# Performance work log

Measured on AMD Instinct MI355X. Metric: run time of the kernel, lower is better.

## Reference

```python
import jax, jax.numpy as jnp
import numpy as np

B, C_IN, C_OUT, F, K = 4, 64, 64, 50000, 16
BN_EPS = 1e-5


def setup_inputs() -> dict:
    key = jax.random.key(0)
    k1, k2, k3, k4 = jax.random.split(key, 4)
    fea = jax.random.normal(k1, (B, C_IN, F), dtype=jnp.float32)
    ring_n = jax.random.randint(k2, (B, F, K), 0, F, dtype=jnp.int64)
    # Conv1d(kernel_size=1) weight [out, in] and bias [out]
    W = jax.random.normal(k3, (C_OUT, C_IN), dtype=jnp.float32) / np.sqrt(C_IN)
    b = jax.random.normal(k4, (C_OUT,), dtype=jnp.float32) * 0.01
    gamma = jnp.ones((C_OUT,), dtype=jnp.float32)
    beta = jnp.zeros((C_OUT,), dtype=jnp.float32)
    return {"fea": fea, "ring_n": ring_n, "W": W, "b": b, "gamma": gamma, "beta": beta}


def reference(fea, ring_n, W, b, gamma, beta):
    # Note: original torch code overwrites the cat result, so only the
    # NEIGHBOR features are summed (center face excluded).
    def gather_sum(f, r):  # f: [C, F], r: [F, K]
        return f[:, r].sum(axis=-1)  # [C, F, K] -> [C, F]

    summed = jax.vmap(gather_sum)(fea, ring_n)  # [B, C_in, F]
    # 1x1 conv == channel matmul
    y = jnp.einsum("oc,bcf->bof", W, summed) + b[None, :, None]  # [B, C_out, F]
    # BatchNorm1d (training mode): stats over (batch, faces) per channel
    mean = y.mean(axis=(0, 2), keepdims=True)
    var = y.var(axis=(0, 2), keepdims=True)  # biased, as torch BN uses for normalization
    y = (y - mean) * jax.lax.rsqrt(var + BN_EPS)
    y = y * gamma[None, :, None] + beta[None, :, None]
    return jax.nn.relu(y)
```

## Files before the change

### kernel.cpp

```cpp
#include <hip/hip_runtime.h>
#include <hip/hip_bf16.h>
#include <stdint.h>

#define Bn 4
#define Cn 64
#define Fn 50000
#define Kn 16
#define NTOT (Bn*Fn)
#define EPS 1e-5f

typedef unsigned short u16;
typedef unsigned int u32;
typedef __attribute__((ext_vector_type(8))) short short8;
typedef __attribute__((ext_vector_type(4))) float f32x4;
typedef __attribute__((ext_vector_type(4))) int i32x4;
typedef __attribute__((ext_vector_type(4))) unsigned int u32x4;

__device__ __forceinline__ u16 f2bf(float x) {
  __hip_bfloat16 h = __float2bfloat16(x);
  return *reinterpret_cast<u16*>(&h);
}
__device__ __forceinline__ u32 pack2(float a, float b) {
  return (u32)f2bf(a) | ((u32)f2bf(b) << 16);
}

__global__ __launch_bounds__(256) void k1_mfma(
    const float* __restrict__ fea, const float* __restrict__ W,
    u32* __restrict__ Gt) {
  const int b = blockIdx.y;
  const int f0 = blockIdx.x * 128;
  const int t = threadIdx.x;
  const int l = t & 63;
  const int quad = l >> 4;
  const int lane15 = l & 15;
  const int wv = t >> 6;
  __shared__ float a_s[64][129];

  short8 afr[4][2];
  #pragma unroll
  for (int ot = 0; ot < 4; ot++) {
    #pragma unroll
    for (int kk = 0; kk < 2; kk++) {
      const float* wr = W + (ot * 16 + lane15) * 64 + kk * 32 + quad * 8;
      float4 wa = *(const float4*)wr;
      float4 wb = *(const float4*)(wr + 4);
      union { short8 v; u32 u[4]; } fr;
      fr.u[0] = pack2(wa.x, wa.y); fr.u[1] = pack2(wa.z, wa.w);
      fr.u[2] = pack2(wb.x, wb.y); fr.u[3] = pack2(wb.z, wb.w);
      afr[ot][kk] = fr.v;
    }
  }

  {
    const float* fb = fea + (size_t)b * Cn * Fn;
    const int f4 = t & 31;
    const int cbase = t >> 5;
    const bool fvalid = (f0 + f4 * 4) < Fn;
    #pragma unroll
    for (int jj = 0; jj < 8; jj++) {
      int c = cbase + jj * 8;
      float4 v = make_float4(0.f, 0.f, 0.f, 0.f);
      if (fvalid) v = *(const float4*)(fb + (size_t)c * Fn + f0 + f4 * 4);
      *(float4*)&a_s[c][f4 * 4] = v;
    }
  }
  __syncthreads();

  f32x4 acc[4][2];
  #pragma unroll
  for (int ot = 0; ot < 4; ot++)
    #pragma unroll
    for (int ft = 0; ft < 2; ft++) acc[ot][ft] = (f32x4){0.f, 0.f, 0.f, 0.f};

  #pragma unroll
  for (int ft = 0; ft < 2; ft++) {
    const int fl = wv * 32 + ft * 16 + lane15;
    float x[16];
    #pragma unroll
    for (int j = 0; j < 8; j++) x[j] = a_s[quad * 8 + j][fl];
    #pragma unroll
    for (int j = 0; j < 8; j++) x[8 + j] = a_s[32 + quad * 8 + j][fl];
    union { short8 s; u32 u[4]; } b0, b1;
    #pragma unroll
    for (int p = 0; p < 4; p++) {
      b0.u[p] = pack2(x[2 * p], x[2 * p + 1]);
      b1.u[p] = pack2(x[8 + 2 * p], x[8 + 2 * p + 1]);
    }
    #pragma unroll
    for (int ot = 0; ot < 4; ot++) {
      acc[ot][ft] = __builtin_amdgcn_mfma_f32_16x16x32_bf16(afr[ot][0], b0.s, acc[ot][ft], 0, 0, 0);
      acc[ot][ft] = __builtin_amdgcn_mfma_f32_16x16x32_bf16(afr[ot][1], b1.s, acc[ot][ft], 0, 0, 0);
    }
  }

  __syncthreads();
  u32* ts = (u32*)&a_s[0][0];
  #pragma unroll
  for (int ot = 0; ot < 4; ot++) {
    #pragma unroll
    for (int ft = 0; ft < 2; ft++) {
      int fl = wv * 32 + ft * 16 + lane15;
      uint2 pv;
      pv.x = pack2(acc[ot][ft][0], acc[ot][ft][1]);
      pv.y = pack2(acc[ot][ft][2], acc[ot][ft][3]);
      *(uint2*)&ts[fl * 36 + ot * 8 + quad * 2] = pv;
    }
  }
  __syncthreads();
  #pragma unroll
  for (int j = 0; j < 4; j++) {
    int o = j * 1024 + t * 4;
    int fl = o >> 5, sl = o & 31;
    if (f0 + fl < Fn) {
      u32x4 vv = *(const u32x4*)&ts[fl * 36 + sl];
      *(u32x4*)(Gt + ((size_t)b * Fn + f0 + fl) * 32 + sl) = vv;
    }
  }
}

template<int WRITE_BF16>
__global__ __launch_bounds__(256) void k2_gather(
    const u32* __restrict__ Gt, const int* __restrict__ ring,
    const float* __restrict__ bias, u32* __restrict__ Y, float* __restrict__ outF,
    float* __restrict__ gsum, float* __restrict__ gsum2) {
  const int bid = blockIdx.x;
  const int b = (bid & 7) >> 1;
  const int sub = ((bid >> 3) << 1) | (bid & 1);
  const int t = threadIdx.x;
  const int gid = t >> 3;
  const int cs = t & 7;
  const int sch = t & 63;
  const int spart = t >> 6;

  __shared__ float y_s[32][65];
  __shared__ float rs[4][64];
  __shared__ float rs2[4][64];

  float bv[8];
  #pragma unroll
  for (int i = 0; i < 8; i++) bv[i] = bias[cs * 8 + i];

  const u32* Gb = Gt + (size_t)b * Fn * 32;
  const int* rb = ring + (size_t)b * Fn * Kn;

  float sacc = 0.f, s2acc = 0.f;
  const int ntiles = (Fn + 31) / 32;

  for (int tile = sub; tile < ntiles; tile += 512) {
    const int fa = tile * 32 + gid;
    const bool valid = fa < Fn;
    float acc[8];
    #pragma unroll
    for (int i = 0; i < 8; i++) acc[i] = 0.f;

    if (valid) {
      const i32x4* rp = (const i32x4*)(rb + (size_t)fa * Kn);
      i32x4 i0 = __builtin_nontemporal_load(&rp[0]);
      i32x4 i1 = __builtin_nontemporal_load(&rp[1]);
      i32x4 i2 = __builtin_nontemporal_load(&rp[2]);
      i32x4 i3 = __builtin_nontemporal_load(&rp[3]);
      int idx[16] = {i0[0],i0[1],i0[2],i0[3], i1[0],i1[1],i1[2],i1[3],
                     i2[0],i2[1],i2[2],i2[3], i3[0],i3[1],i3[2],i3[3]};
      u32x4 v[8];
      #pragma unroll
      for (int k = 0; k < 8; k++)
        v[k] = *(const u32x4*)(Gb + (size_t)idx[k] * 32 + cs * 4);
      #pragma unroll
      for (int k = 0; k < 8; k++) {
        #pragma unroll
        for (int p = 0; p < 4; p++) {
          u32 uu = v[k][p];
          acc[2*p]   += __uint_as_float(uu << 16);
          acc[2*p+1] += __uint_as_float(uu & 0xffff0000u);
        }
      }
      u32x4 w[8];
      #pragma unroll
      for (int k = 0; k < 8; k++)
        w[k] = *(const u32x4*)(Gb + (size_t)idx[8 + k] * 32 + cs * 4);
      #pragma unroll
      for (int k = 0; k < 8; k++) {
        #pragma unroll
        for (int p = 0; p < 4; p++) {
          u32 uu = w[k][p];
          acc[2*p]   += __uint_as_float(uu << 16);
          acc[2*p+1] += __uint_as_float(uu & 0xffff0000u);
        }
      }
    }

    float yv[8];
    #pragma unroll
    for (int i = 0; i < 8; i++) yv[i] = valid ? acc[i] + bv[i] : 0.f;

    if (WRITE_BF16 && valid) {
      u32x4 pv;
      pv[0] = pack2(yv[0], yv[1]); pv[1] = pack2(yv[2], yv[3]);
      pv[2] = pack2(yv[4], yv[5]); pv[3] = pack2(yv[6], yv[7]);
      __builtin_nontemporal_store(pv,
          (u32x4*)(Y + ((size_t)b * Fn + fa) * 32 + cs * 4));
    }

    #pragma unroll
    for (int i = 0; i < 8; i++) y_s[gid][cs * 8 + i] = yv[i];
    __syncthreads();
    #pragma unroll
    for (int i = 0; i < 8; i++) {
      float v = y_s[spart * 8 + i][sch];
      sacc += v; s2acc += v * v;
    }
    if (!WRITE_BF16) {
      const int ch = t >> 2, q = t & 3;
      #pragma unroll
      for (int jj = 0; jj < 2; jj++) {
        int f4 = q + jj * 4;
        int fb = tile * 32 + f4 * 4;
        if (fb < Fn) {
          float4 wv4;
          wv4.x = y_s[f4 * 4 + 0][ch]; wv4.y = y_s[f4 * 4 + 1][ch];
          wv4.z = y_s[f4 * 4 + 2][ch]; wv4.w = y_s[f4 * 4 + 3][ch];
          *(float4*)(outF + ((size_t)b * 64 + ch) * Fn + fb) = wv4;
        }
      }
    }
    __syncthreads();
  }

  rs[spart][sch] = sacc;
  rs2[spart][sch] = s2acc;
  __syncthreads();
  if (t < 64) {
    float s = rs[0][t] + rs[1][t] + rs[2][t] + rs[3][t];
    atomicAdd(&gsum[t], s);
  } else if (t < 128) {
    const int ch = t - 64;
    float s2 = rs2[0][ch] + rs2[1][ch] + rs2[2][ch] + rs2[3][ch];
    atomicAdd(&gsum2[ch], s2);
  }
}

__global__ void k3_stats(const float* __restrict__ gsum, const float* __restrict__ gsum2,
                         const float* __restrict__ gamma, const float* __restrict__ beta,
                         float* __restrict__ ab) {
  int o = threadIdx.x;
  if (o < 64) {
    float inv = 1.0f / (float)NTOT;
    float mean = gsum[o] * inv;
    float var = gsum2[o] * inv - mean * mean;
    float r = rsqrtf(var + EPS);
    float a = gamma[o] * r;
    ab[o] = a;
    ab[64 + o] = beta[o] - mean * a;
  }
}

__global__ __launch_bounds__(256) void k4_norm_bf(
    const u32* __restrict__ Y, const float* __restrict__ gsum,
    const float* __restrict__ gsum2, const float* __restrict__ gamma,
    const float* __restrict__ beta, float* __restrict__ out) {
  const int b = blockIdx.y;
  const int f0 = blockIdx.x * 64;
  const int t = threadIdx.x;
  __shared__ u32 ys[32][65];

  #pragma unroll
  for (int j = 0; j < 2; j++) {
    int o = j * 1024 + t * 4;
    int fl = o >> 5, sl = o & 31;
    u32x4 vv = (u32x4)(0u);
    if (f0 + fl < Fn)
      vv = *(const u32x4*)(Y + ((size_t)b * Fn + f0 + fl) * 32 + sl);
    ys[sl + 0][fl] = vv[0]; ys[sl + 1][fl] = vv[1];
    ys[sl + 2][fl] = vv[2]; ys[sl + 3][fl] = vv[3];
  }
  __syncthreads();

  const float inv = 1.0f / (float)NTOT;
  const int fi = t & 15, g = t >> 4;
  const int fbase = 4 * fi;
  #pragma unroll
  for (int j = 0; j < 4; j++) {
    int ch = g * 4 + j;
    float mean = gsum[ch] * inv;
    float var = gsum2[ch] * inv - mean * mean;
    float a = gamma[ch] * rsqrtf(var + EPS);
    float cc = beta[ch] - mean * a;
    if (f0 + fbase < Fn) {
      const int c2 = ch >> 1;
      const bool hi = ch & 1;
      float r[4];
      #pragma unroll
      for (int rr = 0; rr < 4; rr++) {
        u32 u = ys[c2][fbase + rr];
        float xv = __uint_as_float(hi ? (u & 0xffff0000u) : (u << 16));
        r[rr] = fmaxf(fmaf(xv, a, cc), 0.f);
      }
      float4 res = make_float4(r[0], r[1], r[2], r[3]);
      *(float4*)(out + ((size_t)b * 64 + ch) * Fn + f0 + fbase) = res;
    }
  }
}

__global__ __launch_bounds__(256) void k4_norm_f32(float* __restrict__ out,
                                                   const float* __restrict__ ab) {
  int i = blockIdx.x * 256 + threadIdx.x;
  int o = (i / (Fn / 4)) & 63;
  float a = ab[o], c = ab[64 + o];
  float4 v = ((float4*)out)[i];
  v.x = fmaxf(fmaf(v.x, a, c), 0.f);
  v.y = fmaxf(fmaf(v.y, a, c), 0.f);
  v.z = fmaxf(fmaf(v.z, a, c), 0.f);
  v.w = fmaxf(fmaf(v.w, a, c), 0.f);
  ((float4*)out)[i] = v;
}

extern "C" void kernel_launch(void* const* d_in, const int* in_sizes, int n_in,
                              void* d_out, int out_size, void* d_ws, size_t ws_size,
                              hipStream_t stream) {
  const float* fea   = (const float*)d_in[0];
  const int*   ring  = (const int*)d_in[1];
  const float* W     = (const float*)d_in[2];
  const float* bias  = (const float*)d_in[3];
  const float* gamma = (const float*)d_in[4];
  const float* beta  = (const float*)d_in[5];
  float* out = (float*)d_out;

  u32* Gt = (u32*)d_ws;
  const size_t gtBytes = (size_t)Bn * Fn * 32 * 4;
  const size_t yBytes  = (size_t)Bn * Fn * 32 * 4;
  const bool bf16y = ws_size >= gtBytes + yBytes + 1024;

  u32* Y = Gt + (size_t)Bn * Fn * 32;
  float* gsum  = bf16y ? (float*)((char*)d_ws + gtBytes + yBytes)
                       : (float*)((char*)d_ws + gtBytes);
  float* gsum2 = gsum + 64;
  float* ab    = gsum + 128;

  hipMemsetAsync(gsum, 0, 2 * 64 * sizeof(float), stream);
  k1_mfma<<<dim3((Fn + 127) / 128, Bn), 256, 0, stream>>>(fea, W, Gt);
  if (bf16y) {
    k2_gather<1><<<dim3(2048), 256, 0, stream>>>(Gt, ring, bias, Y, out, gsum, gsum2);
    k4_norm_bf<<<dim3((Fn + 63) / 64, Bn), 256, 0, stream>>>(Y, gsum, gsum2, gamma, beta, out);
  } else {
    k2_gather<0><<<dim3(2048), 256, 0, stream>>>(Gt, ring, bias, Y, out, gsum, gsum2);
    k3_stats<<<1, 64, 0, stream>>>(gsum, gsum2, gamma, beta, ab);
    k4_norm_f32<<<dim3((Bn * Cn * Fn / 4) / 256), 256, 0, stream>>>(out, ab);
  }
}
```

Measured before the change: 204.0 us.

## Prefetch next tile's ring indices and keep BN stats in registers

```diff
diff --git a/kernel.cpp b/kernel.cpp
--- a/kernel.cpp
+++ b/kernel.cpp
@@ -129,12 +129,9 @@
   const int t = threadIdx.x;
   const int gid = t >> 3;
   const int cs = t & 7;
-  const int sch = t & 63;
-  const int spart = t >> 6;
-
-  __shared__ float y_s[32][65];
-  __shared__ float rs[4][64];
-  __shared__ float rs2[4][64];
+
+  __shared__ float rs[32][68];
+  __shared__ float rs2[32][68];
 
   float bv[8];
   #pragma unroll
@@ -143,98 +140,111 @@
   const u32* Gb = Gt + (size_t)b * Fn * 32;
   const int* rb = ring + (size_t)b * Fn * Kn;
 
-  float sacc = 0.f, s2acc = 0.f;
+  float sacc[8], s2acc[8];
+  #pragma unroll
+  for (int i = 0; i < 8; i++) { sacc[i] = 0.f; s2acc[i] = 0.f; }
+
   const int ntiles = (Fn + 31) / 32;
 
-  for (int tile = sub; tile < ntiles; tile += 512) {
+  int tile = sub;
+  i32x4 r0, r1, r2, r3;
+  if (tile < ntiles) {
+    int fa = tile * 32 + gid;
+    int fc = fa < Fn ? fa : Fn - 1;
+    const i32x4* rp = (const i32x4*)(rb + (size_t)fc * Kn);
+    r0 = __builtin_nontemporal_load(&rp[0]);
+    r1 = __builtin_nontemporal_load(&rp[1]);
+    r2 = __builtin_nontemporal_load(&rp[2]);
+    r3 = __builtin_nontemporal_load(&rp[3]);
+  }
+
+  for (; tile < ntiles; tile += 512) {
     const int fa = tile * 32 + gid;
     const bool valid = fa < Fn;
+    int idx[16] = {r0[0],r0[1],r0[2],r0[3], r1[0],r1[1],r1[2],r1[3],
+                   r2[0],r2[1],r2[2],r2[3], r3[0],r3[1],r3[2],r3[3]};
+
+    const int ntile = tile + 512;
+    if (ntile < ntiles) {
+      int nfa = ntile * 32 + gid;
+      int nfc = nfa < Fn ? nfa : Fn - 1;
+      const i32x4* rp = (const i32x4*)(rb + (size_t)nfc * Kn);
+      r0 = __builtin_nontemporal_load(&rp[0]);
+      r1 = __builtin_nontemporal_load(&rp[1]);
+      r2 = __builtin_nontemporal_load(&rp[2]);
+      r3 = __builtin_nontemporal_load(&rp[3]);
+    }
+
     float acc[8];
     #pragma unroll
     for (int i = 0; i < 8; i++) acc[i] = 0.f;
 
+    u32x4 v[8];
+    #pragma unroll
+    for (int k = 0; k < 8; k++)
+      v[k] = *(const u32x4*)(Gb + (size_t)idx[k] * 32 + cs * 4);
+    #pragma unroll
+    for (int k = 0; k < 8; k++) {
+      #pragma unroll
+      for (int p = 0; p < 4; p++) {
+        u32 uu = v[k][p];
+        acc[2*p]   += __uint_as_float(uu << 16);
+        acc[2*p+1] += __uint_as_float(uu & 0xffff0000u);
+      }
+    }
+    #pragma unroll
+    for (int k = 0; k < 8; k++)
+      v[k] = *(const u32x4*)(Gb + (size_t)idx[8 + k] * 32 + cs * 4);
+    #pragma unroll
+    for (int k = 0; k < 8; k++) {
+      #pragma unroll
+      for (int p = 0; p < 4; p++) {
+        u32 uu = v[k][p];
+        acc[2*p]   += __uint_as_float(uu << 16);
+        acc[2*p+1] += __uint_as_float(uu & 0xffff0000u);
+      }
+    }
+
+    float yv[8];
+    #pragma unroll
+    for (int i = 0; i < 8; i++) yv[i] = acc[i] + bv[i];
+
     if (valid) {
-      const i32x4* rp = (const i32x4*)(rb + (size_t)fa * Kn);
-      i32x4 i0 = __builtin_nontemporal_load(&rp[0]);
-      i32x4 i1 = __builtin_nontemporal_load(&rp[1]);
-      i32x4 i2 = __builtin_nontemporal_load(&rp[2]);
-      i32x4 i3 = __builtin_nontemporal_load(&rp[3]);
-      int idx[16] = {i0[0],i0[1],i0[2],i0[3], i1[0],i1[1],i1[2],i1[3],
-                     i2[0],i2[1],i2[2],i2[3], i3[0],i3[1],i3[2],i3[3]};
-      u32x4 v[8];
+      if (WRITE_BF16) {
+        u32x4 pv;
+        pv[0] = pack2(yv[0], yv[1]); pv[1] = pack2(yv[2], yv[3]);
+        pv[2] = pack2(yv[4], yv[5]); pv[3] = pack2(yv[6], yv[7]);
+        __builtin_nontemporal_store(pv,
+            (u32x4*)(Y + ((size_t)b * Fn + fa) * 32 + cs * 4));
+      } else {
+        #pragma unroll
+        for (int i = 0; i < 8; i++)
+          outF[((size_t)b * 64 + cs * 8 + i) * Fn + fa] = yv[i];
+      }
       #pragma unroll
-      for (int k = 0; k < 8; k++)
-        v[k] = *(const u32x4*)(Gb + (size_t)idx[k] * 32 + cs * 4);
-      #pragma unroll
-      for (int k = 0; k < 8; k++) {
-        #pragma unroll
-        for (int p = 0; p < 4; p++) {
-          u32 uu = v[k][p];
-          acc[2*p]   += __uint_as_float(uu << 16);
-          acc[2*p+1] += __uint_as_float(uu & 0xffff0000u);
-        }
-      }
-      u32x4 w[8];
-      #pragma unroll
-      for (int k = 0; k < 8; k++)
-        w[k] = *(const u32x4*)(Gb + (size_t)idx[8 + k] * 32 + cs * 4);
-      #pragma unroll
-      for (int k = 0; k < 8; k++) {
-        #pragma unroll
-        for (int p = 0; p < 4; p++) {
-          u32 uu = w[k][p];
-          acc[2*p]   += __uint_as_float(uu << 16);
-          acc[2*p+1] += __uint_as_float(uu & 0xffff0000u);
-        }
-      }
-    }
-
-    float yv[8];
-    #pragma unroll
-    for (int i = 0; i < 8; i++) yv[i] = valid ? acc[i] + bv[i] : 0.f;
-
-    if (WRITE_BF16 && valid) {
-      u32x4 pv;
-      pv[0] = pack2(yv[0], yv[1]); pv[1] = pack2(yv[2], yv[3]);
-      pv[2] = pack2(yv[4], yv[5]); pv[3] = pack2(yv[6], yv[7]);
-      __builtin_nontemporal_store(pv,
-          (u32x4*)(Y + ((size_t)b * Fn + fa) * 32 + cs * 4));
-    }
-
-    #pragma unroll
-    for (int i = 0; i < 8; i++) y_s[gid][cs * 8 + i] = yv[i];
-    __syncthreads();
-    #pragma unroll
-    for (int i = 0; i < 8; i++) {
-      float v = y_s[spart * 8 + i][sch];
-      sacc += v; s2acc += v * v;
-    }
-    if (!WRITE_BF16) {
-      const int ch = t >> 2, q = t & 3;
-      #pragma unroll
-      for (int jj = 0; jj < 2; jj++) {
-        int f4 = q + jj * 4;
-        int fb = tile * 32 + f4 * 4;
-        if (fb < Fn) {
-          float4 wv4;
-          wv4.x = y_s[f4 * 4 + 0][ch]; wv4.y = y_s[f4 * 4 + 1][ch];
-          wv4.z = y_s[f4 * 4 + 2][ch]; wv4.w = y_s[f4 * 4 + 3][ch];
-          *(float4*)(outF + ((size_t)b * 64 + ch) * Fn + fb) = wv4;
-        }
-      }
-    }
-    __syncthreads();
-  }
-
-  rs[spart][sch] = sacc;
-  rs2[spart][sch] = s2acc;
+      for (int i = 0; i < 8; i++) {
+        sacc[i] += yv[i];
+        s2acc[i] += yv[i] * yv[i];
+      }
+    }
+  }
+
+  #pragma unroll
+  for (int i = 0; i < 8; i++) {
+    rs[gid][cs * 8 + i] = sacc[i];
+    rs2[gid][cs * 8 + i] = s2acc[i];
+  }
   __syncthreads();
   if (t < 64) {
-    float s = rs[0][t] + rs[1][t] + rs[2][t] + rs[3][t];
+    float s = 0.f;
+    #pragma unroll
+    for (int g = 0; g < 32; g++) s += rs[g][t];
     atomicAdd(&gsum[t], s);
   } else if (t < 128) {
     const int ch = t - 64;
-    float s2 = rs2[0][ch] + rs2[1][ch] + rs2[2][ch] + rs2[3][ch];
+    float s2 = 0.f;
+    #pragma unroll
+    for (int g = 0; g < 32; g++) s2 += rs2[g][ch];
     atomicAdd(&gsum2[ch], s2);
   }
 }
```

Result: no change. 202.5 us (-0.7%).
